# Performance work log

Measured on AMD Instinct MI355X. Metric: run time of the kernel, lower is better.

The kernel has to match this reference:

```python
import jax, jax.numpy as jnp
import numpy as np
from jax import lax

D_VECTOR = 128
N_SUB = 8
D_SUB = 16          # d_vector // n_subvectors
N_CLUSTERS = 256
N_CODEBOOKS = 64
N_DATA = 131072
CHUNK = 1024        # data chunk for gather-compute-scatter (keeps gathered codebook small)


def setup_inputs() -> dict:
    key = jax.random.key(0)
    k1, k2, k3 = jax.random.split(key, 3)
    x = jax.random.normal(k1, (D_VECTOR, N_DATA), dtype=jnp.float32)
    codebook = jax.random.normal(k2, (N_CODEBOOKS, N_SUB, D_SUB, N_CLUSTERS), dtype=jnp.float32)
    selector_centroids = jax.random.normal(k3, (D_VECTOR, N_CODEBOOKS), dtype=jnp.float32)
    return {"x": x, "codebook": codebook, "selector_centroids": selector_centroids}


def _predict_labels(x, centroids):
    # x: [D, N], centroids: [D, L] -> squared euclidean distance [N, L], argmin -> [N]
    d = (jnp.sum(x * x, axis=0)[:, None]
         - 2.0 * (x.T @ centroids)
         + jnp.sum(centroids * centroids, axis=0)[None, :])
    return jnp.argmin(d, axis=1)


def reference(x, codebook, selector_centroids):
    N = x.shape[1]
    # 1) codebook_selector.predict -> per-point codebook label
    labels = _predict_labels(x, selector_centroids)          # [N] int
    # 2) split into subvectors (same layout as torch reshape of [d_vector, n]):
    x_sub = x.reshape(N_SUB, D_SUB, N)                       # [S, d, N]
    nchunks = N // CHUNK
    xc = x_sub.reshape(N_SUB, D_SUB, nchunks, CHUNK).transpose(2, 0, 1, 3)  # [nc, S, d, C]
    lc = labels.reshape(nchunks, CHUNK)                      # [nc, C]

    def body(args):
        xch, lch = args                                      # [S, d, C], [C]
        cb = codebook[lch]                                   # gather: [C, S, d, K]
        cross = jnp.einsum('sdc,csdk->sck', xch, cb)
        cnorm = jnp.sum(cb * cb, axis=2).transpose(1, 0, 2)  # [S, C, K]
        xnorm = jnp.sum(xch * xch, axis=1)[..., None]        # [S, C, 1]
        dist = xnorm - 2.0 * cross + cnorm
        code = jnp.argmin(dist, axis=2)                      # [S, C] (PQ codes, 0..255)
        # decode: gather chosen centroid per (point, subvector)
        idx = code.T[:, :, None, None]                       # [C, S, 1, 1]
        recon = jnp.take_along_axis(cb, idx, axis=3)[..., 0] # [C, S, d]
        return recon.transpose(1, 2, 0)                      # [S, d, C]

    recon = lax.map(body, (xc, lc))                          # [nc, S, d, C]
    recon = recon.transpose(1, 2, 0, 3).reshape(D_VECTOR, N) # [d_vector, N]
    return recon
```

## Files before the change

### kernel.cpp

```cpp
#include <hip/hip_runtime.h>

#define N_DATA     131072
#define D_VECTOR   128
#define N_SUB      8
#define D_SUB      16
#define N_CLUSTERS 256
#define N_CODEBOOKS 64

typedef float v2f __attribute__((ext_vector_type(2)));

#define WS_LABELS 0
#define WS_PERM   (N_DATA)
#define WS_CNT    (2*N_DATA)
#define WS_CURSOR (2*N_DATA + 64)
#define WS_OFF    (2*N_DATA + 128)
#define WS_CNORM  (2*N_DATA + 256)
#define WS_CNSEL  (WS_CNORM + N_CODEBOOKS*N_SUB*N_CLUSTERS)
#define WS_CODES  (WS_CNSEL + 64)
#define WS_CBT2   (WS_CODES + 262144)
#define CBT2_WORDS (N_CODEBOOKS*N_SUB*N_CLUSTERS*D_SUB)

__global__ __launch_bounds__(256) void pq_precompute(
    const float* __restrict__ cb, const float* __restrict__ sel,
    float* __restrict__ cnorm_cb, float* __restrict__ cnorm_sel,
    float* __restrict__ cbT2, int* __restrict__ cnt)
{
    int row = blockIdx.x;
    int k   = threadIdx.x;
    const float* p = cb + (size_t)row * (D_SUB * N_CLUSTERS) + k;
    float vals[D_SUB];
    float sum = 0.f;
#pragma unroll
    for (int d = 0; d < D_SUB; d++) {
        float v = p[(size_t)d * N_CLUSTERS];
        vals[d] = v;
        sum = __fadd_rn(sum, __fmul_rn(v, v));
    }
    int idx = row * 256 + k;
    cnorm_cb[idx] = sum;
    if (cbT2) {
        float4* dst = (float4*)(cbT2 + ((size_t)row << 12) + ((size_t)k << 4));
#pragma unroll
        for (int q = 0; q < 4; q++)
            dst[q] = make_float4(vals[4*q], vals[4*q+1], vals[4*q+2], vals[4*q+3]);
    }
    if (idx < N_CODEBOOKS) {
        float s2 = 0.f;
        for (int d = 0; d < D_VECTOR; d++) {
            float v = sel[d * N_CODEBOOKS + idx];
            s2 = __fadd_rn(s2, __fmul_rn(v, v));
        }
        cnorm_sel[idx] = s2;
        cnt[idx] = 0;
    }
}

__global__ __launch_bounds__(256, 4) void pq_labels2(
    const float* __restrict__ x, const float* __restrict__ sel,
    const float* __restrict__ cnorm_sel,
    int* __restrict__ labels, int* __restrict__ cnt)
{
    __shared__ int hist[N_CODEBOOKS];
    int tid = threadIdx.x;
    if (tid < N_CODEBOOKS) hist[tid] = 0;
    __syncthreads();

    int n = blockIdx.x * 256 + tid;

    v2f acc[32];
#pragma unroll
    for (int lp = 0; lp < 32; lp++) acc[lp] = (v2f){0.f, 0.f};

    float xn = 0.f;
    for (int d = 0; d < D_VECTOR; d++) {
        float xv = x[(size_t)d * N_DATA + n];
        xn = __fadd_rn(xn, __fmul_rn(xv, xv));
        v2f xv2 = (v2f){xv, xv};
        const v2f* sp = (const v2f*)(sel + d * N_CODEBOOKS);
#pragma unroll
        for (int lp = 0; lp < 32; lp++)
            acc[lp] = __builtin_elementwise_fma(xv2, sp[lp], acc[lp]);
    }

    float best = 1e30f;
    int   bl = 0;
#pragma unroll
    for (int lp = 0; lp < 32; lp++) {
        float dx = __fadd_rn(__fsub_rn(xn, __fmul_rn(2.0f, acc[lp].x)), cnorm_sel[2*lp]);
        float dy = __fadd_rn(__fsub_rn(xn, __fmul_rn(2.0f, acc[lp].y)), cnorm_sel[2*lp + 1]);
        if (dx < best) { best = dx; bl = 2*lp; }
        if (dy < best) { best = dy; bl = 2*lp + 1; }
    }
    labels[n] = bl;
    atomicAdd(&hist[bl], 1);
    __syncthreads();
    if (tid < N_CODEBOOKS) atomicAdd(&cnt[tid], hist[tid]);
}

__global__ void pq_scan(const int* __restrict__ cnt, int* __restrict__ off, int* __restrict__ cursor)
{
    int tid = threadIdx.x;
    int v = cnt[tid];
    int inc = v;
#pragma unroll
    for (int sft = 1; sft < 64; sft <<= 1) {
        int o = __shfl_up(inc, sft, 64);
        if (tid >= sft) inc += o;
    }
    int exc = inc - v;
    off[tid] = exc;
    cursor[tid] = exc;
    if (tid == 63) off[64] = inc;
}

__global__ __launch_bounds__(256) void pq_scatter(
    const float* __restrict__ x, const int* __restrict__ labels,
    int* __restrict__ cursor, unsigned int* __restrict__ perm,
    float* __restrict__ xg)
{
    __shared__ int lcnt[N_CODEBOOKS];
    __shared__ int lbase[N_CODEBOOKS];
    int tid = threadIdx.x;
    if (tid < N_CODEBOOKS) lcnt[tid] = 0;
    __syncthreads();
    int base = blockIdx.x * 1024;
    int lv[4], slot[4];
#pragma unroll
    for (int i = 0; i < 4; i++) {
        int n = base + i * 256 + tid;
        int l = labels[n];
        lv[i] = l;
        slot[i] = atomicAdd(&lcnt[l], 1);
    }
    __syncthreads();
    if (tid < N_CODEBOOKS) lbase[tid] = atomicAdd(&cursor[tid], lcnt[tid]);
    __syncthreads();
#pragma unroll
    for (int i = 0; i < 4; i++) {
        int n = base + i * 256 + tid;
        int dst = lbase[lv[i]] + slot[i];
        perm[dst] = ((unsigned)n << 6) | (unsigned)lv[i];
#pragma unroll
        for (int s = 0; s < N_SUB; s++) {
            float v[D_SUB];
#pragma unroll
            for (int d = 0; d < D_SUB; d++)
                v[d] = x[(size_t)(s * D_SUB + d) * N_DATA + n];
            float4* o = (float4*)(xg + (((size_t)s * N_DATA + (size_t)dst) << 4));
            o[0] = make_float4(v[0],  v[1],  v[2],  v[3]);
            o[1] = make_float4(v[4],  v[5],  v[6],  v[7]);
            o[2] = make_float4(v[8],  v[9],  v[10], v[11]);
            o[3] = make_float4(v[12], v[13], v[14], v[15]);
        }
    }
}

__global__ __launch_bounds__(256, 8) void pq_encode9(
    const float* __restrict__ xg, const float* __restrict__ cb,
    const float* __restrict__ cnorm_cb, const unsigned int* __restrict__ perm,
    unsigned char* __restrict__ codes)
{
    int tid = threadIdx.x;
    int s   = blockIdx.x & 7;
    int pos = (int)(blockIdx.x >> 3) * 256 + tid;
    unsigned pk = perm[pos];
    int n = (int)(pk >> 6);
    int l = (int)(pk & 63u);

    const float4* xp = (const float4*)(xg + (((size_t)s * N_DATA + (size_t)pos) << 4));
    float4 x0 = xp[0], x1 = xp[1], x2 = xp[2], x3 = xp[3];
    float xs[D_SUB] = { x0.x, x0.y, x0.z, x0.w, x1.x, x1.y, x1.z, x1.w,
                        x2.x, x2.y, x2.z, x2.w, x3.x, x3.y, x3.z, x3.w };

    float xn = 0.f;
#pragma unroll
    for (int d = 0; d < D_SUB; d++)
        xn = __fadd_rn(xn, __fmul_rn(xs[d], xs[d]));

    v2f xs2[D_SUB];
#pragma unroll
    for (int d = 0; d < D_SUB; d++) xs2[d] = (v2f){xs[d], xs[d]};
    const v2f xnv  = (v2f){xn, xn};
    const v2f twov = (v2f){2.f, 2.f};

    int bestk = 0;
    bool done = false;
    while (true) {
        unsigned long long todo = __ballot(!done);
        if (!todo) break;
        int src  = (int)(__ffsll((long long)todo) - 1);
        int lcur = __builtin_amdgcn_readlane(l, src);

        const float* cbs = cb       + ((size_t)(lcur * N_SUB + s) << 12);
        const float* cns = cnorm_cb + ((size_t)(lcur * N_SUB + s) << 8);

        float bx = 1e30f, by = 1e30f;
        int   kx = 0, ky = 0;
        {
#pragma clang fp contract(off)
#pragma unroll 2
            for (int kkp = 0; kkp < N_CLUSTERS / 2; kkp++) {
                v2f cn2 = *(const v2f*)(cns + (kkp << 1));
                v2f a = (v2f){0.f, 0.f};
#pragma unroll
                for (int d = 0; d < D_SUB; d++) {
                    v2f c = *(const v2f*)(cbs + (size_t)(d * N_CLUSTERS) + (kkp << 1));
                    a = a + xs2[d] * c;
                }
                v2f dd = (xnv - twov * a) + cn2;
                if (dd.x < bx) { bx = dd.x; kx = kkp; }
                if (dd.y < by) { by = dd.y; ky = kkp; }
            }
        }
        int bk = 2 * kx;
        { int kodd = 2 * ky + 1; if (by < bx || (by == bx && kodd < bk)) bk = kodd; }

        if (!done && l == lcur) { bestk = bk; done = true; }
    }
    codes[((size_t)n << 3) | s] = (unsigned char)bestk;
}

__global__ __launch_bounds__(256) void pq_decode_fast(
    const float* __restrict__ cbT2, const int* __restrict__ labels,
    const unsigned char* __restrict__ codes, float* __restrict__ out)
{
    int s = blockIdx.x & 7;
    int n = (blockIdx.x >> 3) * 256 + threadIdx.x;
    int l = labels[n];
    int k = codes[(size_t)n * N_SUB + s];
    const float4* p = (const float4*)(cbT2 + ((size_t)(l * N_SUB + s) << 12) + ((size_t)k << 4));
    float4 a = p[0], b = p[1], c = p[2], d = p[3];
    float v[D_SUB] = { a.x, a.y, a.z, a.w, b.x, b.y, b.z, b.w,
                       c.x, c.y, c.z, c.w, d.x, d.y, d.z, d.w };
#pragma unroll
    for (int dd = 0; dd < D_SUB; dd++)
        out[(size_t)(s * D_SUB + dd) * N_DATA + n] = v[dd];
}

__global__ __launch_bounds__(256) void pq_decode(
    const float* __restrict__ cb, const int* __restrict__ labels,
    const unsigned char* __restrict__ codes, float* __restrict__ out)
{
    int s = blockIdx.x & 7;
    int n = (blockIdx.x >> 3) * 256 + threadIdx.x;
    int l = labels[n];
    int k = codes[(size_t)n * N_SUB + s];
    const float* base = cb + ((size_t)(l * N_SUB + s) * D_SUB) * N_CLUSTERS + k;
#pragma unroll
    for (int dd = 0; dd < D_SUB; dd++)
        out[(size_t)(s * D_SUB + dd) * N_DATA + n] = base[(size_t)dd * N_CLUSTERS];
}

extern "C" void kernel_launch(void* const* d_in, const int* in_sizes, int n_in,
                              void* d_out, int out_size, void* d_ws, size_t ws_size,
                              hipStream_t stream)
{
    (void)in_sizes; (void)n_in; (void)out_size;
    const float* x   = (const float*)d_in[0];
    const float* cb  = (const float*)d_in[1];
    const float* sel = (const float*)d_in[2];
    float* out = (float*)d_out;

    int*   wsi    = (int*)d_ws;
    float* wsf    = (float*)d_ws;
    int*   labels = wsi + WS_LABELS;
    unsigned int* perm = (unsigned int*)(wsi + WS_PERM);
    int*   cnt    = wsi + WS_CNT;
    int*   cursor = wsi + WS_CURSOR;
    int*   off    = wsi + WS_OFF;
    float* cnorm  = wsf + WS_CNORM;
    float* cnsel  = wsf + WS_CNSEL;
    unsigned char* codes = (unsigned char*)(wsi + WS_CODES);

    bool big = ws_size >= (size_t)(WS_CBT2 + CBT2_WORDS) * 4u;
    float* cbT2 = big ? (wsf + WS_CBT2) : (float*)nullptr;

    float* xg = out;

    hipLaunchKernelGGL(pq_precompute, dim3(512), dim3(256), 0, stream, cb, sel, cnorm, cnsel, cbT2, cnt);
    hipLaunchKernelGGL(pq_labels2, dim3(N_DATA / 256), dim3(256), 0, stream, x, sel, cnsel, labels, cnt);
    hipLaunchKernelGGL(pq_scan, dim3(1), dim3(64), 0, stream, cnt, off, cursor);
    hipLaunchKernelGGL(pq_scatter, dim3(N_DATA / 1024), dim3(256), 0, stream, x, labels, cursor, perm, xg);
    hipLaunchKernelGGL(pq_encode9, dim3((N_DATA / 256) * N_SUB), dim3(256), 0, stream,
                       xg, cb, cnorm, perm, codes);
    if (big)
        hipLaunchKernelGGL(pq_decode_fast, dim3((N_DATA / 256) * N_SUB), dim3(256), 0, stream,
                           cbT2, labels, codes, out);
    else
        hipLaunchKernelGGL(pq_decode, dim3((N_DATA / 256) * N_SUB), dim3(256), 0, stream,
                           cb, labels, codes, out);
}
```

Baseline: 430.2 us.

## Add two-point-per-thread encode kernel with pair-interleaved transposed codebook

Changes the precomputed transposed codebook to a layout where pairs of clusters are interleaved per dimension, so encode can load contiguous v2f vectors for two clusters at once. A new encode kernel processes two points per thread, reusing each loaded codebook pair for both points, and double-buffers the codebook registers across the cluster loop. Decode reads the new strided layout. This aims to halve codebook loads per point and overlap loads with compute, at the cost of higher register pressure, lower occupancy, and strided decode reads.

```diff
diff --git a/kernel.cpp b/kernel.cpp
--- a/kernel.cpp
+++ b/kernel.cpp
@@ -17,33 +17,27 @@
 #define WS_CNORM  (2*N_DATA + 256)
 #define WS_CNSEL  (WS_CNORM + N_CODEBOOKS*N_SUB*N_CLUSTERS)
 #define WS_CODES  (WS_CNSEL + 64)
-#define WS_CBT2   (WS_CODES + 262144)
-#define CBT2_WORDS (N_CODEBOOKS*N_SUB*N_CLUSTERS*D_SUB)
+#define WS_CBT    (WS_CODES + 262144)
+#define CBT_WORDS (N_CODEBOOKS*N_SUB*N_CLUSTERS*D_SUB)
 
 __global__ __launch_bounds__(256) void pq_precompute(
     const float* __restrict__ cb, const float* __restrict__ sel,
     float* __restrict__ cnorm_cb, float* __restrict__ cnorm_sel,
-    float* __restrict__ cbT2, int* __restrict__ cnt)
+    float* __restrict__ cbT, int* __restrict__ cnt)
 {
     int row = blockIdx.x;
     int k   = threadIdx.x;
     const float* p = cb + (size_t)row * (D_SUB * N_CLUSTERS) + k;
-    float vals[D_SUB];
+    float* ct = cbT ? cbT + ((size_t)row << 12) + ((size_t)(k >> 1) << 5) + (k & 1) : (float*)0;
     float sum = 0.f;
 #pragma unroll
     for (int d = 0; d < D_SUB; d++) {
         float v = p[(size_t)d * N_CLUSTERS];
-        vals[d] = v;
+        if (ct) ct[d << 1] = v;
         sum = __fadd_rn(sum, __fmul_rn(v, v));
     }
     int idx = row * 256 + k;
     cnorm_cb[idx] = sum;
-    if (cbT2) {
-        float4* dst = (float4*)(cbT2 + ((size_t)row << 12) + ((size_t)k << 4));
-#pragma unroll
-        for (int q = 0; q < 4; q++)
-            dst[q] = make_float4(vals[4*q], vals[4*q+1], vals[4*q+2], vals[4*q+3]);
-    }
     if (idx < N_CODEBOOKS) {
         float s2 = 0.f;
         for (int d = 0; d < D_VECTOR; d++) {
@@ -153,6 +147,111 @@
             o[3] = make_float4(v[12], v[13], v[14], v[15]);
         }
     }
+}
+
+__global__ __launch_bounds__(256, 6) void pq_encode10(
+    const float* __restrict__ xg, const float* __restrict__ cbT,
+    const float* __restrict__ cnorm_cb, const unsigned int* __restrict__ perm,
+    unsigned char* __restrict__ codes)
+{
+    int tid  = threadIdx.x;
+    int lane = tid & 63;
+    int w    = tid >> 6;
+    int s    = blockIdx.x & 7;
+    int base = (int)(blockIdx.x >> 3) * 512 + w * 128;
+    int pos0 = base + lane;
+    int pos1 = pos0 + 64;
+
+    unsigned pk0 = perm[pos0], pk1 = perm[pos1];
+    int n0 = (int)(pk0 >> 6), l0 = (int)(pk0 & 63u);
+    int n1 = (int)(pk1 >> 6), l1 = (int)(pk1 & 63u);
+
+    const float4* xp0 = (const float4*)(xg + (((size_t)s * N_DATA + (size_t)pos0) << 4));
+    const float4* xp1 = (const float4*)(xg + (((size_t)s * N_DATA + (size_t)pos1) << 4));
+    float4 a0 = xp0[0], a1 = xp0[1], a2 = xp0[2], a3 = xp0[3];
+    float4 b0 = xp1[0], b1 = xp1[1], b2 = xp1[2], b3 = xp1[3];
+    float xsA[D_SUB] = { a0.x,a0.y,a0.z,a0.w, a1.x,a1.y,a1.z,a1.w,
+                         a2.x,a2.y,a2.z,a2.w, a3.x,a3.y,a3.z,a3.w };
+    float xsB[D_SUB] = { b0.x,b0.y,b0.z,b0.w, b1.x,b1.y,b1.z,b1.w,
+                         b2.x,b2.y,b2.z,b2.w, b3.x,b3.y,b3.z,b3.w };
+
+    float xn0 = 0.f, xn1 = 0.f;
+#pragma unroll
+    for (int d = 0; d < D_SUB; d++) {
+        xn0 = __fadd_rn(xn0, __fmul_rn(xsA[d], xsA[d]));
+        xn1 = __fadd_rn(xn1, __fmul_rn(xsB[d], xsB[d]));
+    }
+
+    v2f xs20[D_SUB], xs21[D_SUB];
+#pragma unroll
+    for (int d = 0; d < D_SUB; d++) { xs20[d] = (v2f){xsA[d], xsA[d]}; xs21[d] = (v2f){xsB[d], xsB[d]}; }
+    const v2f xnv0 = (v2f){xn0, xn0}, xnv1 = (v2f){xn1, xn1};
+    const v2f twov = (v2f){2.f, 2.f};
+
+    bool d0 = false, d1 = false;
+    int bk0 = 0, bk1 = 0;
+
+    while (true) {
+        unsigned long long todo = __ballot(!d0 || !d1);
+        if (!todo) break;
+        int src  = (int)(__ffsll((long long)todo) - 1);
+        int lsel = (!d0) ? l0 : l1;
+        int lcur = __builtin_amdgcn_readlane(lsel, src);
+
+        const v2f* cbp = (const v2f*)(cbT      + ((size_t)(lcur * N_SUB + s) << 12));
+        const v2f* cnp = (const v2f*)(cnorm_cb + ((size_t)(lcur * N_SUB + s) << 8));
+
+        float b0x = 1e30f, b0y = 1e30f, b1x = 1e30f, b1y = 1e30f;
+        int   k0x = 0, k0y = 0, k1x = 0, k1y = 0;
+        {
+#pragma clang fp contract(off)
+            v2f cA[16], cB[16], cnA, cnB;
+            cnA = cnp[0];
+#pragma unroll
+            for (int j = 0; j < 16; j++) cA[j] = cbp[j];
+
+#define PQ_COMP(CREG, CNREG, KKP)                                              \
+            do {                                                               \
+                v2f q0 = (v2f){0.f, 0.f}, q1 = (v2f){0.f, 0.f};                \
+                _Pragma("unroll")                                              \
+                for (int d = 0; d < D_SUB; d++) {                              \
+                    v2f c = CREG[d];                                           \
+                    q0 = q0 + xs20[d] * c;         \
+                    q1 = q1 + xs21[d] * c;                                     \
+                }                                                              \
+                v2f e0 = (xnv0 - twov * q0) + CNREG;                           \
+                v2f e1 = (xnv1 - twov * q1) + CNREG;                           \
+                if (e0.x < b0x) { b0x = e0.x; k0x = (KKP); }                   \
+                if (e0.y < b0y) { b0y = e0.y; k0y = (KKP); }                   \
+                if (e1.x < b1x) { b1x = e1.x; k1x = (KKP); }                   \
+                if (e1.y < b1y) { b1y = e1.y; k1y = (KKP); }                   \
+            } while (0)
+
+#pragma clang loop unroll(disable)
+            for (int kk = 0; kk < N_CLUSTERS / 2; kk += 2) {
+                cnB = cnp[kk + 1];
+#pragma unroll
+                for (int j = 0; j < 16; j++) cB[j] = cbp[(kk + 1) * 16 + j];
+                PQ_COMP(cA, cnA, kk);
+                if (kk + 2 < N_CLUSTERS / 2) {
+                    cnA = cnp[kk + 2];
+#pragma unroll
+                    for (int j = 0; j < 16; j++) cA[j] = cbp[(kk + 2) * 16 + j];
+                }
+                PQ_COMP(cB, cnB, kk + 1);
+            }
+#undef PQ_COMP
+        }
+        int m0 = 2 * k0x;
+        { int ko = 2 * k0y + 1; if (b0y < b0x || (b0y == b0x && ko < m0)) m0 = ko; }
+        int m1 = 2 * k1x;
+        { int ko = 2 * k1y + 1; if (b1y < b1x || (b1y == b1x && ko < m1)) m1 = ko; }
+
+        if (!d0 && l0 == lcur) { bk0 = m0; d0 = true; }
+        if (!d1 && l1 == lcur) { bk1 = m1; d1 = true; }
+    }
+    codes[((size_t)n0 << 3) | s] = (unsigned char)bk0;
+    codes[((size_t)n1 << 3) | s] = (unsigned char)bk1;
 }
 
 __global__ __launch_bounds__(256, 8) void pq_encode9(
@@ -221,17 +320,17 @@
 }
 
 __global__ __launch_bounds__(256) void pq_decode_fast(
-    const float* __restrict__ cbT2, const int* __restrict__ labels,
+    const float* __restrict__ cbT, const int* __restrict__ labels,
     const unsigned char* __restrict__ codes, float* __restrict__ out)
 {
     int s = blockIdx.x & 7;
     int n = (blockIdx.x >> 3) * 256 + threadIdx.x;
     int l = labels[n];
     int k = codes[(size_t)n * N_SUB + s];
-    const float4* p = (const float4*)(cbT2 + ((size_t)(l * N_SUB + s) << 12) + ((size_t)k << 4));
-    float4 a = p[0], b = p[1], c = p[2], d = p[3];
-    float v[D_SUB] = { a.x, a.y, a.z, a.w, b.x, b.y, b.z, b.w,
-                       c.x, c.y, c.z, c.w, d.x, d.y, d.z, d.w };
+    const float* base = cbT + ((size_t)(l * N_SUB + s) << 12) + ((size_t)(k >> 1) << 5) + (k & 1);
+    float v[D_SUB];
+#pragma unroll
+    for (int dd = 0; dd < D_SUB; dd++) v[dd] = base[dd << 1];
 #pragma unroll
     for (int dd = 0; dd < D_SUB; dd++)
         out[(size_t)(s * D_SUB + dd) * N_DATA + n] = v[dd];
@@ -272,21 +371,24 @@
     float* cnsel  = wsf + WS_CNSEL;
     unsigned char* codes = (unsigned char*)(wsi + WS_CODES);
 
-    bool big = ws_size >= (size_t)(WS_CBT2 + CBT2_WORDS) * 4u;
-    float* cbT2 = big ? (wsf + WS_CBT2) : (float*)nullptr;
+    bool big = ws_size >= (size_t)(WS_CBT + CBT_WORDS) * 4u;
+    float* cbT = big ? (wsf + WS_CBT) : (float*)nullptr;
 
     float* xg = out;
 
-    hipLaunchKernelGGL(pq_precompute, dim3(512), dim3(256), 0, stream, cb, sel, cnorm, cnsel, cbT2, cnt);
+    hipLaunchKernelGGL(pq_precompute, dim3(512), dim3(256), 0, stream, cb, sel, cnorm, cnsel, cbT, cnt);
     hipLaunchKernelGGL(pq_labels2, dim3(N_DATA / 256), dim3(256), 0, stream, x, sel, cnsel, labels, cnt);
     hipLaunchKernelGGL(pq_scan, dim3(1), dim3(64), 0, stream, cnt, off, cursor);
     hipLaunchKernelGGL(pq_scatter, dim3(N_DATA / 1024), dim3(256), 0, stream, x, labels, cursor, perm, xg);
-    hipLaunchKernelGGL(pq_encode9, dim3((N_DATA / 256) * N_SUB), dim3(256), 0, stream,
-                       xg, cb, cnorm, perm, codes);
-    if (big)
+    if (big) {
+        hipLaunchKernelGGL(pq_encode10, dim3((N_DATA / 512) * N_SUB), dim3(256), 0, stream,
+                           xg, cbT, cnorm, perm, codes);
         hipLaunchKernelGGL(pq_decode_fast, dim3((N_DATA / 256) * N_SUB), dim3(256), 0, stream,
-                           cbT2, labels, codes, out);
-    else
+                           cbT, labels, codes, out);
+    } else {
+        hipLaunchKernelGGL(pq_encode9, dim3((N_DATA / 256) * N_SUB), dim3(256), 0, stream,
+                           xg, cb, cnorm, perm, codes);
         hipLaunchKernelGGL(pq_decode, dim3((N_DATA / 256) * N_SUB), dim3(256), 0, stream,
                            cb, labels, codes, out);
-}
+    }
+}
```

New measurement: 1.709 ms. +297.2%, slower.

## Stage per-label codebook slice in LDS for block-wide reuse in encode

Applied to the files above, without the earlier changes.

The encode kernel now uses the label range of each 256-point block. Points are sorted by label, so that range runs from the first thread's label to the last. For each label in that range the block cooperatively loads the 16x256 sub-codebook and its norms into shared memory, then only the matching threads compute distances. This replaces the per-wavefront ballot loop that read the codebook straight from global memory or cache. The inner loop is also widened to four clusters per iteration using float4 LDS reads, and launch bounds drop to 4 blocks per unit. The cost is extra barriers, LDS usage and lower occupancy, and non-matching threads sit idle while each label is processed.

```diff
diff --git a/kernel.cpp b/kernel.cpp
--- a/kernel.cpp
+++ b/kernel.cpp
@@ -155,11 +155,15 @@
     }
 }
 
-__global__ __launch_bounds__(256, 8) void pq_encode9(
+__global__ __launch_bounds__(256, 4) void pq_encode13(
     const float* __restrict__ xg, const float* __restrict__ cb,
     const float* __restrict__ cnorm_cb, const unsigned int* __restrict__ perm,
     unsigned char* __restrict__ codes)
 {
+    __shared__ float s_cb[D_SUB * N_CLUSTERS];
+    __shared__ float s_cn[N_CLUSTERS];
+    __shared__ int   s_l0, s_l1;
+
     int tid = threadIdx.x;
     int s   = blockIdx.x & 7;
     int pos = (int)(blockIdx.x >> 3) * 256 + tid;
@@ -167,6 +171,9 @@
     int n = (int)(pk >> 6);
     int l = (int)(pk & 63u);
 
+    if (tid == 0)   s_l0 = l;
+    if (tid == 255) s_l1 = l;
+
     const float4* xp = (const float4*)(xg + (((size_t)s * N_DATA + (size_t)pos) << 4));
     float4 x0 = xp[0], x1 = xp[1], x2 = xp[2], x3 = xp[3];
     float xs[D_SUB] = { x0.x, x0.y, x0.z, x0.w, x1.x, x1.y, x1.z, x1.w,
@@ -183,41 +190,51 @@
     const v2f xnv  = (v2f){xn, xn};
     const v2f twov = (v2f){2.f, 2.f};
 
-    int bestk = 0;
-    bool done = false;
-    while (true) {
-        unsigned long long todo = __ballot(!done);
-        if (!todo) break;
-        int src  = (int)(__ffsll((long long)todo) - 1);
-        int lcur = __builtin_amdgcn_readlane(l, src);
-
-        const float* cbs = cb       + ((size_t)(lcur * N_SUB + s) << 12);
-        const float* cns = cnorm_cb + ((size_t)(lcur * N_SUB + s) << 8);
-
-        float bx = 1e30f, by = 1e30f;
-        int   kx = 0, ky = 0;
+    __syncthreads();
+    int l0 = s_l0, l1 = s_l1;
+
+    float bx = 1e30f, by = 1e30f;
+    int   kx = 0, ky = 0;
+
+    for (int lcur = l0; lcur <= l1; ++lcur) {
         {
+            const float4* src = (const float4*)(cb + (size_t)(lcur * N_SUB + s) * (D_SUB * N_CLUSTERS));
+            float4* d4 = (float4*)s_cb;
+#pragma unroll
+            for (int i = 0; i < 4; i++) d4[i * 256 + tid] = src[i * 256 + tid];
+            if (tid < 64)
+                ((float4*)s_cn)[tid] = ((const float4*)(cnorm_cb + ((size_t)(lcur * N_SUB + s) << 8)))[tid];
+        }
+        __syncthreads();
+
+        if (l == lcur) {
 #pragma clang fp contract(off)
 #pragma unroll 2
-            for (int kkp = 0; kkp < N_CLUSTERS / 2; kkp++) {
-                v2f cn2 = *(const v2f*)(cns + (kkp << 1));
-                v2f a = (v2f){0.f, 0.f};
+            for (int k4 = 0; k4 < N_CLUSTERS / 4; k4++) {
+                float4 cnq = *(const float4*)(s_cn + (k4 << 2));
+                v2f a0 = (v2f){0.f, 0.f}, a1 = (v2f){0.f, 0.f};
 #pragma unroll
                 for (int d = 0; d < D_SUB; d++) {
-                    v2f c = *(const v2f*)(cbs + (size_t)(d * N_CLUSTERS) + (kkp << 1));
-                    a = a + xs2[d] * c;
+                    float4 c = *(const float4*)(s_cb + d * N_CLUSTERS + (k4 << 2));
+                    v2f clo = (v2f){c.x, c.y};
+                    v2f chi = (v2f){c.z, c.w};
+                    a0 = a0 + xs2[d] * clo;
+                    a1 = a1 + xs2[d] * chi;
                 }
-                v2f dd = (xnv - twov * a) + cn2;
-                if (dd.x < bx) { bx = dd.x; kx = kkp; }
-                if (dd.y < by) { by = dd.y; ky = kkp; }
+                v2f d0 = (xnv - twov * a0) + (v2f){cnq.x, cnq.y};
+                v2f d1 = (xnv - twov * a1) + (v2f){cnq.z, cnq.w};
+                if (d0.x < bx) { bx = d0.x; kx = (k4 << 2); }
+                if (d1.x < bx) { bx = d1.x; kx = (k4 << 2) + 2; }
+                if (d0.y < by) { by = d0.y; ky = (k4 << 2) + 1; }
+                if (d1.y < by) { by = d1.y; ky = (k4 << 2) + 3; }
             }
         }
-        int bk = 2 * kx;
-        { int kodd = 2 * ky + 1; if (by < bx || (by == bx && kodd < bk)) bk = kodd; }
-
-        if (!done && l == lcur) { bestk = bk; done = true; }
-    }
-    codes[((size_t)n << 3) | s] = (unsigned char)bestk;
+        __syncthreads();
+    }
+
+    int bk = kx;
+    if (by < bx || (by == bx && ky < kx)) bk = ky;
+    codes[((size_t)n << 3) | s] = (unsigned char)bk;
 }
 
 __global__ __launch_bounds__(256) void pq_decode_fast(
@@ -281,7 +298,7 @@
     hipLaunchKernelGGL(pq_labels2, dim3(N_DATA / 256), dim3(256), 0, stream, x, sel, cnsel, labels, cnt);
     hipLaunchKernelGGL(pq_scan, dim3(1), dim3(64), 0, stream, cnt, off, cursor);
     hipLaunchKernelGGL(pq_scatter, dim3(N_DATA / 1024), dim3(256), 0, stream, x, labels, cursor, perm, xg);
-    hipLaunchKernelGGL(pq_encode9, dim3((N_DATA / 256) * N_SUB), dim3(256), 0, stream,
+    hipLaunchKernelGGL(pq_encode13, dim3((N_DATA / 256) * N_SUB), dim3(256), 0, stream,
                        xg, cb, cnorm, perm, codes);
     if (big)
         hipLaunchKernelGGL(pq_decode_fast, dim3((N_DATA / 256) * N_SUB), dim3(256), 0, stream,
```

After: 465.0 us. +8.1%, slower.

## Restructure PQ encode: lanes split clusters, codebook in registers, DPP min reduction

Applied to the files above, without the earlier changes.

The encode kernel no longer gives each lane one point that scans all 256 clusters with wave-uniform codebook loads. Each wave now processes 64 sorted points one at a time. Every lane holds 4 clusters of the current codebook in registers and reloads them only when the label changes, and a DPP/readlane min-reduction plus a ballot picks the argmin. The point norms move into the scatter kernel and are read back through a new workspace buffer, and the next point's data is double-buffered. In exchange there are more cross-lane reduction instructions per point and lower occupancy (launch bounds 3). Ties resolve to the lowest lane, which keeps the lowest-index semantics.

```diff
diff --git a/kernel.cpp b/kernel.cpp
--- a/kernel.cpp
+++ b/kernel.cpp
@@ -17,7 +17,8 @@
 #define WS_CNORM  (2*N_DATA + 256)
 #define WS_CNSEL  (WS_CNORM + N_CODEBOOKS*N_SUB*N_CLUSTERS)
 #define WS_CODES  (WS_CNSEL + 64)
-#define WS_CBT2   (WS_CODES + 262144)
+#define WS_XN8P   (WS_CODES + 262144)
+#define WS_CBT2   (WS_XN8P + N_SUB*N_DATA)
 #define CBT2_WORDS (N_CODEBOOKS*N_SUB*N_CLUSTERS*D_SUB)
 
 __global__ __launch_bounds__(256) void pq_precompute(
@@ -116,7 +117,7 @@
 __global__ __launch_bounds__(256) void pq_scatter(
     const float* __restrict__ x, const int* __restrict__ labels,
     int* __restrict__ cursor, unsigned int* __restrict__ perm,
-    float* __restrict__ xg)
+    float* __restrict__ xg, float* __restrict__ xn8p)
 {
     __shared__ int lcnt[N_CODEBOOKS];
     __shared__ int lbase[N_CODEBOOKS];
@@ -151,73 +152,124 @@
             o[1] = make_float4(v[4],  v[5],  v[6],  v[7]);
             o[2] = make_float4(v[8],  v[9],  v[10], v[11]);
             o[3] = make_float4(v[12], v[13], v[14], v[15]);
-        }
-    }
-}
-
-__global__ __launch_bounds__(256, 8) void pq_encode9(
+            float xn = 0.f;
+#pragma unroll
+            for (int d = 0; d < D_SUB; d++)
+                xn = __fadd_rn(xn, __fmul_rn(v[d], v[d]));
+            xn8p[(size_t)s * N_DATA + (size_t)dst] = xn;
+        }
+    }
+}
+
+template<int CTRL>
+__device__ __forceinline__ float dppmin(float v)
+{
+    int t = __builtin_amdgcn_update_dpp(__float_as_int(v), __float_as_int(v),
+                                        CTRL, 0xF, 0xF, false);
+    return fminf(v, __int_as_float(t));
+}
+
+__global__ __launch_bounds__(256, 3) void pq_encode14(
     const float* __restrict__ xg, const float* __restrict__ cb,
-    const float* __restrict__ cnorm_cb, const unsigned int* __restrict__ perm,
-    unsigned char* __restrict__ codes)
-{
-    int tid = threadIdx.x;
-    int s   = blockIdx.x & 7;
-    int pos = (int)(blockIdx.x >> 3) * 256 + tid;
-    unsigned pk = perm[pos];
-    int n = (int)(pk >> 6);
-    int l = (int)(pk & 63u);
-
-    const float4* xp = (const float4*)(xg + (((size_t)s * N_DATA + (size_t)pos) << 4));
-    float4 x0 = xp[0], x1 = xp[1], x2 = xp[2], x3 = xp[3];
-    float xs[D_SUB] = { x0.x, x0.y, x0.z, x0.w, x1.x, x1.y, x1.z, x1.w,
-                        x2.x, x2.y, x2.z, x2.w, x3.x, x3.y, x3.z, x3.w };
-
-    float xn = 0.f;
-#pragma unroll
-    for (int d = 0; d < D_SUB; d++)
-        xn = __fadd_rn(xn, __fmul_rn(xs[d], xs[d]));
-
-    v2f xs2[D_SUB];
-#pragma unroll
-    for (int d = 0; d < D_SUB; d++) xs2[d] = (v2f){xs[d], xs[d]};
-    const v2f xnv  = (v2f){xn, xn};
-    const v2f twov = (v2f){2.f, 2.f};
-
-    int bestk = 0;
-    bool done = false;
-    while (true) {
-        unsigned long long todo = __ballot(!done);
-        if (!todo) break;
-        int src  = (int)(__ffsll((long long)todo) - 1);
-        int lcur = __builtin_amdgcn_readlane(l, src);
-
-        const float* cbs = cb       + ((size_t)(lcur * N_SUB + s) << 12);
-        const float* cns = cnorm_cb + ((size_t)(lcur * N_SUB + s) << 8);
-
-        float bx = 1e30f, by = 1e30f;
-        int   kx = 0, ky = 0;
+    const float* __restrict__ cnorm_cb, const float* __restrict__ xn8p,
+    const unsigned int* __restrict__ perm, unsigned char* __restrict__ codes)
+{
+    int tid  = threadIdx.x;
+    int lane = tid & 63;
+    int w    = tid >> 6;
+    int s    = blockIdx.x & 7;
+    int base = (int)(blockIdx.x >> 3) * 256 + w * 64;
+
+    int lcur = -1;
+    v2f cbA[D_SUB], cbB[D_SUB];
+    v2f cnA = (v2f){0.f, 0.f}, cnB = (v2f){0.f, 0.f};
+    int mycode = 0, myn = 0;
+
+    unsigned pkc = perm[base];
+    float4 xbuf[2][4];
+    float  xnbuf[2];
+    {
+        const float4* xp = (const float4*)(xg + (((size_t)s * N_DATA + (size_t)base) << 4));
+        xbuf[0][0] = xp[0]; xbuf[0][1] = xp[1]; xbuf[0][2] = xp[2]; xbuf[0][3] = xp[3];
+        xnbuf[0] = xn8p[(size_t)s * N_DATA + (size_t)base];
+    }
+    unsigned pkn = perm[base + 1];
+
+#pragma unroll 2
+    for (int i = 0; i < 64; i++) {
+        const int cur = i & 1;
+        const int nxt = cur ^ 1;
+        unsigned pk = pkc;
+        int n = (int)(pk >> 6), l = (int)(pk & 63u);
+
+        if (i < 63) {
+            int posn = base + i + 1;
+            const float4* xq = (const float4*)(xg + (((size_t)s * N_DATA + (size_t)posn) << 4));
+            xbuf[nxt][0] = xq[0]; xbuf[nxt][1] = xq[1];
+            xbuf[nxt][2] = xq[2]; xbuf[nxt][3] = xq[3];
+            xnbuf[nxt] = xn8p[(size_t)s * N_DATA + (size_t)posn];
+        }
+        pkc = pkn;
+        if (i < 62) pkn = perm[base + i + 2];
+
+        if (l != lcur) {
+            lcur = l;
+            const float* cbs = cb + (size_t)(l * N_SUB + s) * (D_SUB * N_CLUSTERS);
+#pragma unroll
+            for (int d = 0; d < D_SUB; d++) {
+                float4 v = *(const float4*)(cbs + (size_t)d * N_CLUSTERS + lane * 4);
+                cbA[d] = (v2f){v.x, v.y};
+                cbB[d] = (v2f){v.z, v.w};
+            }
+            float4 c = *(const float4*)(cnorm_cb + (size_t)(l * N_SUB + s) * N_CLUSTERS + lane * 4);
+            cnA = (v2f){c.x, c.y};
+            cnB = (v2f){c.z, c.w};
+        }
+
+        float4 x0 = xbuf[cur][0], x1 = xbuf[cur][1], x2 = xbuf[cur][2], x3 = xbuf[cur][3];
+        float xs[D_SUB] = { x0.x, x0.y, x0.z, x0.w, x1.x, x1.y, x1.z, x1.w,
+                            x2.x, x2.y, x2.z, x2.w, x3.x, x3.y, x3.z, x3.w };
+        float xn = xnbuf[cur];
+
+        float m; int j;
         {
 #pragma clang fp contract(off)
-#pragma unroll 2
-            for (int kkp = 0; kkp < N_CLUSTERS / 2; kkp++) {
-                v2f cn2 = *(const v2f*)(cns + (kkp << 1));
-                v2f a = (v2f){0.f, 0.f};
-#pragma unroll
-                for (int d = 0; d < D_SUB; d++) {
-                    v2f c = *(const v2f*)(cbs + (size_t)(d * N_CLUSTERS) + (kkp << 1));
-                    a = a + xs2[d] * c;
-                }
-                v2f dd = (xnv - twov * a) + cn2;
-                if (dd.x < bx) { bx = dd.x; kx = kkp; }
-                if (dd.y < by) { by = dd.y; ky = kkp; }
+            v2f a0 = (v2f){0.f, 0.f}, a1 = (v2f){0.f, 0.f};
+#pragma unroll
+            for (int d = 0; d < D_SUB; d++) {
+                v2f xv = (v2f){xs[d], xs[d]};
+                a0 = a0 + xv * cbA[d];
+                a1 = a1 + xv * cbB[d];
             }
-        }
-        int bk = 2 * kx;
-        { int kodd = 2 * ky + 1; if (by < bx || (by == bx && kodd < bk)) bk = kodd; }
-
-        if (!done && l == lcur) { bestk = bk; done = true; }
-    }
-    codes[((size_t)n << 3) | s] = (unsigned char)bestk;
+            v2f xnv  = (v2f){xn, xn};
+            v2f twov = (v2f){2.f, 2.f};
+            v2f d0 = (xnv - twov * a0) + cnA;
+            v2f d1 = (xnv - twov * a1) + cnB;
+
+            m = fminf(fminf(d0.x, d0.y), fminf(d1.x, d1.y));
+            j = (d1.x == m) ? 2 : 3;
+            j = (d0.y == m) ? 1 : j;
+            j = (d0.x == m) ? 0 : j;
+        }
+
+        float g = m;
+        g = dppmin<0x111>(g);
+        g = dppmin<0x112>(g);
+        g = dppmin<0x114>(g);
+        g = dppmin<0x118>(g);
+        g = dppmin<0x142>(g);
+        g = dppmin<0x143>(g);
+        float gmin = __int_as_float(__builtin_amdgcn_readlane(__float_as_int(g), 63));
+
+        unsigned long long bal = __ballot(m == gmin);
+        int winner = (int)(__ffsll((long long)bal) - 1);
+        int myk = (lane << 2) | j;
+        int kwin = __builtin_amdgcn_readlane(myk, winner);
+        bool selp = (lane == i);
+        mycode = selp ? kwin : mycode;
+        myn    = selp ? n    : myn;
+    }
+    codes[((size_t)myn << 3) | s] = (unsigned char)mycode;
 }
 
 __global__ __launch_bounds__(256) void pq_decode_fast(
@@ -271,6 +323,7 @@
     float* cnorm  = wsf + WS_CNORM;
     float* cnsel  = wsf + WS_CNSEL;
     unsigned char* codes = (unsigned char*)(wsi + WS_CODES);
+    float* xn8p   = wsf + WS_XN8P;
 
     bool big = ws_size >= (size_t)(WS_CBT2 + CBT2_WORDS) * 4u;
     float* cbT2 = big ? (wsf + WS_CBT2) : (float*)nullptr;
@@ -280,9 +333,9 @@
     hipLaunchKernelGGL(pq_precompute, dim3(512), dim3(256), 0, stream, cb, sel, cnorm, cnsel, cbT2, cnt);
     hipLaunchKernelGGL(pq_labels2, dim3(N_DATA / 256), dim3(256), 0, stream, x, sel, cnsel, labels, cnt);
     hipLaunchKernelGGL(pq_scan, dim3(1), dim3(64), 0, stream, cnt, off, cursor);
-    hipLaunchKernelGGL(pq_scatter, dim3(N_DATA / 1024), dim3(256), 0, stream, x, labels, cursor, perm, xg);
-    hipLaunchKernelGGL(pq_encode9, dim3((N_DATA / 256) * N_SUB), dim3(256), 0, stream,
-                       xg, cb, cnorm, perm, codes);
+    hipLaunchKernelGGL(pq_scatter, dim3(N_DATA / 1024), dim3(256), 0, stream, x, labels, cursor, perm, xg, xn8p);
+    hipLaunchKernelGGL(pq_encode14, dim3((N_DATA / 256) * N_SUB), dim3(256), 0, stream,
+                       xg, cb, cnorm, xn8p, perm, codes);
     if (big)
         hipLaunchKernelGGL(pq_decode_fast, dim3((N_DATA / 256) * N_SUB), dim3(256), 0, stream,
                            cbT2, labels, codes, out);
```

New measurement: 478.7 us. +11.3%, slower.
